# Performance work log

Hardware: AMD Instinct MI355X
Metric: run time of the kernel (lower is better)

## Reference

```python
import jax, jax.numpy as jnp
import numpy as np

B, S, D, H, DFF, L = 32, 512, 512, 8, 2048, 3
DK = D // H
NEG = -1e32


def _ln(x, g, b):
    m = jnp.mean(x, axis=-1, keepdims=True)
    v = jnp.mean((x - m) ** 2, axis=-1, keepdims=True)
    return (x - m) / jnp.sqrt(v + 1e-5) * g + b


def _mha(query, key, value, mask, zero_pad, gam, Wk, bk, Wv, bv, Wo, bo):
    # kq_same: q and k both use k_linear
    q = (query @ Wk + bk).reshape(B, S, H, DK).transpose(0, 2, 1, 3)
    k = (key @ Wk + bk).reshape(B, S, H, DK).transpose(0, 2, 1, 3)
    v = (value @ Wv + bv).reshape(B, S, H, DK).transpose(0, 2, 1, 3)
    scores = jnp.einsum('bhid,bhjd->bhij', q, k) / jnp.sqrt(jnp.float32(DK))
    # distance-decay rescoring (no-grad in original)
    p = jax.nn.softmax(jnp.where(mask, scores, NEG), axis=-1) * mask
    distcum = jnp.cumsum(p, axis=-1)
    disttotal = jnp.sum(p, axis=-1, keepdims=True)
    idx = jnp.arange(S)
    pos = jnp.abs(idx[None, :] - idx[:, None]).astype(jnp.float32)  # [S,S]
    dist = jax.lax.stop_gradient(
        jnp.sqrt(jnp.clip((disttotal - distcum) * pos[None, None], 0.0, None)))
    gamma = -jax.nn.softplus(gam)[None, :, None, None]  # [1,H,1,1]
    total_effect = jnp.clip(jnp.exp(dist * gamma), 1e-5, 1e5)
    scores = jnp.where(mask, scores * total_effect, NEG)
    scores = jax.nn.softmax(scores, axis=-1)
    if zero_pad:
        scores = scores * (idx[:, None] > 0)[None, None, :, :].astype(scores.dtype) * 0 + \
                 scores * (idx > 0).astype(scores.dtype)[None, None, :, None]
    out = jnp.einsum('bhij,bhjd->bhid', scores, v)
    out = out.transpose(0, 2, 1, 3).reshape(B, S, D)
    return out @ Wo + bo


def _layer(i, mask, zero_pad, query, key, values, apply_pos,
           Wk, bk, Wv, bv, Wo, bo, gammas, ln1_g, ln1_b, W1, b1, W2, b2, ln2_g, ln2_b):
    a = _mha(query, key, values, mask, zero_pad, gammas[i],
             Wk[i], bk[i], Wv[i], bv[i], Wo[i], bo[i])
    x = _ln(query + a, ln1_g[i], ln1_b[i])
    if apply_pos:
        f = jax.nn.relu(x @ W1[i] + b1[i]) @ W2[i] + b2[i]
        x = _ln(x + f, ln2_g[i], ln2_b[i])
    return x


def setup_inputs() -> dict:
    key = jax.random.key(0)
    ks = jax.random.split(key, 12)
    sc = 0.02
    inp = {
        'q_embed_data': jax.random.normal(ks[0], (B, S, D), jnp.float32),
        'qa_embed_data': jax.random.normal(ks[1], (B, S, D), jnp.float32),
        'Wk': jax.random.normal(ks[2], (L, D, D), jnp.float32) * sc,
        'bk': jnp.zeros((L, D), jnp.float32),
        'Wv': jax.random.normal(ks[3], (L, D, D), jnp.float32) * sc,
        'bv': jnp.zeros((L, D), jnp.float32),
        'Wo': jax.random.normal(ks[4], (L, D, D), jnp.float32) * sc,
        'bo': jnp.zeros((L, D), jnp.float32),
        'gammas': jax.random.normal(ks[5], (L, H), jnp.float32) * 0.5,
        'ln1_g': jnp.ones((L, D), jnp.float32),
        'ln1_b': jnp.zeros((L, D), jnp.float32),
        'W1': jax.random.normal(ks[6], (L, D, DFF), jnp.float32) * sc,
        'b1': jnp.zeros((L, DFF), jnp.float32),
        'W2': jax.random.normal(ks[7], (L, DFF, D), jnp.float32) * sc,
        'b2': jnp.zeros((L, D), jnp.float32),
        'ln2_g': jnp.ones((L, D), jnp.float32),
        'ln2_b': jnp.zeros((L, D), jnp.float32),
    }
    return inp


def reference(q_embed_data, qa_embed_data, Wk, bk, Wv, bv, Wo, bo, gammas,
              ln1_g, ln1_b, W1, b1, W2, b2, ln2_g, ln2_b):
    P = (Wk, bk, Wv, bv, Wo, bo, gammas, ln1_g, ln1_b, W1, b1, W2, b2, ln2_g, ln2_b)
    mask1 = jnp.tril(jnp.ones((S, S), bool), 0)[None, None]   # peek current+past
    mask0 = jnp.tril(jnp.ones((S, S), bool), -1)[None, None]  # peek only past
    y = qa_embed_data
    x = q_embed_data
    # blocks_1 (n_blocks=1): mask=1, self-attn, apply_pos
    y = _layer(0, mask1, False, y, y, y, True, *P)
    # blocks_2 (2 layers): first mask=1 no FFN, second mask=0 zero_pad cross-attn to y
    x = _layer(1, mask1, False, x, x, x, False, *P)
    x = _layer(2, mask0, True, x, x, y, True, *P)
    return x
```

## Files before the change

kernel.cpp:

```cpp
#include <hip/hip_runtime.h>

#define BB   32
#define SS   512
#define DDIM 512
#define HH   8
#define DFFN 2048
#define MR   (BB*SS)

typedef unsigned int   u32;
typedef unsigned short u16;
typedef unsigned char  u8;
typedef __attribute__((ext_vector_type(8))) short bf16x8;
typedef __attribute__((ext_vector_type(4))) float f32x4;

__device__ __forceinline__ u32 packbf2(float x, float y) {
  u32 ux = __float_as_uint(x), uy = __float_as_uint(y);
  u32 hx = (ux + 0x7FFFu + ((ux >> 16) & 1u)) >> 16;
  u32 hy = (uy + 0x7FFFu + ((uy >> 16) & 1u)) >> 16;
  return hx | (hy << 16);
}
__device__ __forceinline__ u16 pack1bf(float x) {
  u32 u = __float_as_uint(x);
  return (u16)((u + 0x7FFFu + ((u >> 16) & 1u)) >> 16);
}

__device__ __forceinline__ float redsum2(float v) {
  v += __shfl_xor(v, 16, 64);
  v += __shfl_xor(v, 32, 64);
  return v;
}

#if __has_builtin(__builtin_amdgcn_exp2f)
__device__ __forceinline__ float ex2c(float x) { return __builtin_amdgcn_exp2f(fminf(x, 110.f)); }
__device__ __forceinline__ float ex2r(float x) { return __builtin_amdgcn_exp2f(x); }
#else
__device__ __forceinline__ float ex2c(float x) {
  float r = fminf(x, 110.f);
  asm("v_exp_f32 %0, %1" : "=v"(r) : "v"(r));
  return r;
}
__device__ __forceinline__ float ex2r(float x) {
  float r;
  asm("v_exp_f32 %0, %1" : "=v"(r) : "v"(x));
  return r;
}
#endif

__global__ __launch_bounds__(256) void pack_flat2(
    const float* __restrict__ in0, const float* __restrict__ in1,
    u16* __restrict__ out0, u16* __restrict__ out1) {
  const float* in = blockIdx.y ? in1 : in0;
  u16* out = blockIdx.y ? out1 : out0;
  size_t i = ((size_t)blockIdx.x * 256 + threadIdx.x) * 8;
  float4 a = *(const float4*)(in + i);
  float4 b = *(const float4*)(in + i + 4);
  uint4 o;
  o.x = packbf2(a.x, a.y); o.y = packbf2(a.z, a.w);
  o.z = packbf2(b.x, b.y); o.w = packbf2(b.z, b.w);
  *(uint4*)(out + i) = o;
}

__device__ __forceinline__ void wtp_body(const float* __restrict__ in,
                                         u16* __restrict__ out, int K, int N,
                                         int bx, int by) {
  __shared__ float tile[64][65];
  const int t  = threadIdx.x;
  const int n0 = bx * 64, k0 = by * 64;
  #pragma unroll
  for (int it = 0; it < 4; ++it) {
    int idx = it * 256 + t;
    int kk = idx >> 4, n4 = idx & 15;
    float4 v = *(const float4*)(in + (size_t)(k0 + kk) * N + n0 + n4 * 4);
    tile[kk][n4*4+0] = v.x; tile[kk][n4*4+1] = v.y;
    tile[kk][n4*4+2] = v.z; tile[kk][n4*4+3] = v.w;
  }
  __syncthreads();
  #pragma unroll
  for (int it = 0; it < 4; ++it) {
    int idx = it * 256 + t;
    int nn = idx >> 4, g = idx & 15;
    uint2 o;
    o.x = packbf2(tile[g*4+0][nn], tile[g*4+1][nn]);
    o.y = packbf2(tile[g*4+2][nn], tile[g*4+3][nn]);
    *(uint2*)(out + (size_t)(n0 + nn) * K + k0 + g * 4) = o;
  }
}
__global__ __launch_bounds__(256) void pack_w_t(const float* __restrict__ in,
                                                u16* __restrict__ out, int K, int N) {
  wtp_body(in + (size_t)blockIdx.z * K * N, out + (size_t)blockIdx.z * N * K,
           K, N, blockIdx.x, blockIdx.y);
}
__global__ __launch_bounds__(256) void pack_w_sq(
    const float* __restrict__ Wk, const float* __restrict__ Wv,
    const float* __restrict__ Wo,
    u16* __restrict__ WkT, u16* __restrict__ WvT, u16* __restrict__ WoT) {
  const int z = blockIdx.z, which = z / 3, li = z % 3;
  const float* in = (which == 0 ? Wk : which == 1 ? Wv : Wo) + (size_t)li * 262144;
  u16* out = (which == 0 ? WkT : which == 1 ? WvT : WoT) + (size_t)li * 262144;
  wtp_body(in, out, 512, 512, blockIdx.x, blockIdx.y);
}

struct GJob { const u16* A; const u16* Bt; const float* bias;
              float* outF; u16* outB; float sc; };
struct GJobs { GJob j[4]; };

__global__ __launch_bounds__(512, 2) void gemm8(
    GJobs jobs, int lda, int ldb, int ldc, int Kz, int relu)
{
  __shared__ __align__(16) u8 lds[131072];

  const GJob J = jobs.j[blockIdx.z];
  const u16* A    = J.A;
  const u16* Bt   = J.Bt;
  const float* bias = J.bias;
  float* outF = J.outF;
  u16*   outB = J.outB;
  const float sc = J.sc;

  const int nwg  = gridDim.x * gridDim.y;
  const int orig = blockIdx.y * gridDim.x + blockIdx.x;
  const int q8   = nwg >> 3, r8 = nwg & 7;
  const int xcd  = orig & 7, idx8 = orig >> 3;
  const int wg   = (xcd < r8 ? xcd * (q8 + 1) : r8 * (q8 + 1) + (xcd - r8) * q8) + idx8;
  const int bx   = wg % gridDim.x, by = wg / gridDim.x;
  const int row0 = by * 256, col0 = bx * 256;

  const int t    = threadIdx.x;
  const int lane = t & 63, wid = t >> 6;
  const int wm   = wid >> 2, wn = wid & 3;
  const int rl   = lane & 15, kg = lane >> 4;

  const int NT = Kz >> 6;

  f32x4 acc[8][4] = {};

  auto stageA = [&](int buf, int h, int kt) {
    #pragma unroll
    for (int l = 0; l < 2; ++l) {
      int s  = (l * 512 + t) >> 3;
      int kb = ((lane & 7) * 16) ^ ((s & 7) << 4);
      int row = row0 + ((s >> 6) * 128) + h * 64 + (s & 63);
      const u8* src = (const u8*)A + (size_t)row * lda * 2 + (size_t)kt * 128 + kb;
      u8* dst = lds + buf * 65536 + h * 16384 + (l * 512 + wid * 64) * 16;
      __builtin_amdgcn_global_load_lds(
          (const __attribute__((address_space(1))) u32*)src,
          (__attribute__((address_space(3))) u32*)dst, 16, 0, 0);
    }
  };
  auto stageB = [&](int buf, int h, int kt) {
    #pragma unroll
    for (int l = 0; l < 2; ++l) {
      int s  = (l * 512 + t) >> 3;
      int kb = ((lane & 7) * 16) ^ ((s & 7) << 4);
      int col = col0 + ((s >> 5) * 64) + h * 32 + (s & 31);
      const u8* src = (const u8*)Bt + (size_t)col * ldb * 2 + (size_t)kt * 128 + kb;
      u8* dst = lds + buf * 65536 + 32768 + h * 16384 + (l * 512 + wid * 64) * 16;
      __builtin_amdgcn_global_load_lds(
          (const __attribute__((address_space(1))) u32*)src,
          (__attribute__((address_space(3))) u32*)dst, 16, 0, 0);
    }
  };

  auto rdA = [&](int buf, int mh, int m, int ks) -> bf16x8 {
    int s = wm * 64 + m * 16 + rl;
    int off = buf * 65536 + mh * 16384 + s * 128 + (((ks * 32 + kg * 8) * 2) ^ ((s & 7) << 4));
    return *(const bf16x8*)(lds + off);
  };
  auto rdB = [&](int buf, int nh, int n, int ks) -> bf16x8 {
    int s = wn * 32 + n * 16 + rl;
    int off = buf * 65536 + 32768 + nh * 16384 + s * 128 + (((ks * 32 + kg * 8) * 2) ^ ((s & 7) << 4));
    return *(const bf16x8*)(lds + off);
  };

#define GBAR asm volatile("s_barrier" ::: "memory")
#define VMW4 asm volatile("s_waitcnt vmcnt(4)" ::: "memory")
#define VMW0 asm volatile("s_waitcnt vmcnt(0)" ::: "memory")

#define PHASE(BUF, MH, NH, STAGECODE, DOVM) do {                               \
    bf16x8 af_[4][2], bf_[2][2];                                               \
    _Pragma("unroll") for (int m_ = 0; m_ < 4; ++m_)                           \
      _Pragma("unroll") for (int k_ = 0; k_ < 2; ++k_)                         \
        af_[m_][k_] = rdA(BUF, MH, m_, k_);                                    \
    _Pragma("unroll") for (int n_ = 0; n_ < 2; ++n_)                           \
      _Pragma("unroll") for (int k_ = 0; k_ < 2; ++k_)                         \
        bf_[n_][k_] = rdB(BUF, NH, n_, k_);                                    \
    STAGECODE;                                                                 \
    if (DOVM == 1) VMW4;                                                       \
    if (DOVM == 2) VMW0;                                                       \
    GBAR;                                                                      \
    __builtin_amdgcn_s_setprio(1);                                             \
    _Pragma("unroll") for (int m_ = 0; m_ < 4; ++m_)                           \
      _Pragma("unroll") for (int n_ = 0; n_ < 2; ++n_) {                       \
        acc[(MH)*4+m_][(NH)*2+n_] = __builtin_amdgcn_mfma_f32_16x16x32_bf16(   \
            af_[m_][0], bf_[n_][0], acc[(MH)*4+m_][(NH)*2+n_], 0, 0, 0);       \
        acc[(MH)*4+m_][(NH)*2+n_] = __builtin_amdgcn_mfma_f32_16x16x32_bf16(   \
            af_[m_][1], bf_[n_][1], acc[(MH)*4+m_][(NH)*2+n_], 0, 0, 0);       \
      }                                                                        \
    __builtin_amdgcn_s_setprio(0);                                             \
    GBAR;                                                                      \
  } while (0)

  stageA(0, 0, 0); stageB(0, 0, 0); stageA(0, 1, 0); stageB(0, 1, 0);
  stageA(1, 0, 1); stageB(1, 0, 1);
  VMW4; GBAR;

  for (int i = 0; i < (NT >> 1) - 1; ++i) {
    const int T1 = 2 * i + 1, T2 = 2 * i + 2, T3 = 2 * i + 3;
    PHASE(0, 0, 0, stageA(1, 1, T1), 0);
    PHASE(0, 0, 1, stageB(1, 1, T1), 0);
    PHASE(0, 1, 0, stageA(0, 0, T2), 0);
    PHASE(0, 1, 1, stageB(0, 0, T2), 1);
    PHASE(1, 0, 0, stageA(0, 1, T2), 0);
    PHASE(1, 0, 1, stageB(0, 1, T2), 0);
    PHASE(1, 1, 0, stageA(1, 0, T3), 0);
    PHASE(1, 1, 1, stageB(1, 0, T3), 1);
  }
  PHASE(0, 0, 0, stageA(1, 1, NT - 1), 0);
  PHASE(0, 0, 1, stageB(1, 1, NT - 1), 0);
  PHASE(0, 1, 0, ;, 0);
  PHASE(0, 1, 1, ;, 2);
  PHASE(1, 0, 0, ;, 0);
  PHASE(1, 0, 1, ;, 0);
  PHASE(1, 1, 0, ;, 0);
  PHASE(1, 1, 1, ;, 0);
#undef PHASE
#undef GBAR
#undef VMW4
#undef VMW0

  #pragma unroll
  for (int M = 0; M < 8; ++M) {
    #pragma unroll
    for (int N2 = 0; N2 < 4; ++N2) {
      const int col = col0 + wn * 64 + N2 * 16 + rl;
      const float bs = bias ? bias[col] : 0.f;
      #pragma unroll
      for (int q = 0; q < 4; ++q) {
        const int row = row0 + wm * 128 + M * 16 + kg * 4 + q;
        float v = (acc[M][N2][q] + bs) * sc;
        if (relu) v = fmaxf(v, 0.f);
        if (outF) outF[(size_t)row * ldc + col] = v;
        if (outB) outB[(size_t)row * ldc + col] = pack1bf(v);
      }
    }
  }
}

__global__ __attribute__((amdgpu_flat_work_group_size(1024, 1024)))
void attn_mfma(
    const u16* __restrict__ qkA, const u16* __restrict__ vbA,
    const float* __restrict__ gmA, u16* __restrict__ outAp,
    const u16* __restrict__ qkB, const u16* __restrict__ vbB,
    const float* __restrict__ gmB, u16* __restrict__ outBp,
    int nA, int mask_excl, int zero_pad)
{
  __shared__ __align__(16) u8 kSb[65536];
  __shared__ __align__(16) u8 vTb[65536];
  __shared__ __align__(16) u8 pChb[16384];

  const int t    = threadIdx.x;
  const int lane = t & 63, wid = t >> 6;
  const int ql   = lane & 15, g = lane >> 4;
  const int bid  = blockIdx.x;
  const int sel  = bid >= nA;
  const u16* qk    = sel ? qkB : qkA;
  const u16* vbuf  = sel ? vbB : vbA;
  const float* gam = sel ? gmB : gmA;
  u16* out         = sel ? outBp : outAp;
  const int bh = sel ? bid - nA : bid;
  const int b = bh >> 3, h = bh & 7;
  const size_t base = (size_t)b * SS * DDIM + (size_t)h * 64;

  float gv = gam[h];
  float sp = (gv > 0.f) ? (gv + log1pf(__expf(-gv))) : log1pf(__expf(gv));
  const float gamma2 = -sp * 1.442695041f;

  for (int it = 0; it < 4; ++it) {
    int idx = it * 1024 + t;
    int j = idx >> 3, u = idx & 7;
    uint4 w = *(const uint4*)(qk + base + (size_t)j * DDIM + u * 8);
    *(uint4*)(kSb + ((j * 128 + u * 16) ^ ((j & 7) << 4))) = w;
  }
  for (int it = 0; it < 2; ++it) {
    int idx = it * 1024 + t;
    int jp = idx >> 3, u = idx & 7;
    const u16* src = vbuf + base + (size_t)(2 * jp) * DDIM + u * 8;
    uint4 r0 = *(const uint4*)src;
    uint4 r1 = *(const uint4*)(src + DDIM);
    const u16* a0 = (const u16*)&r0;
    const u16* a1 = (const u16*)&r1;
    #pragma unroll
    for (int dd = 0; dd < 8; ++dd) {
      int d = u * 8 + dd;
      u32 w = (u32)a0[dd] | ((u32)a1[dd] << 16);
      *(u32*)(vTb + d * 1024 + ((4 * jp) ^ ((dd ^ u) << 4))) = w;
    }
  }
  __syncthreads();

  bool vm[4];
  #pragma unroll
  for (int rg = 0; rg < 4; ++rg) {
    int kl = 4 * g + rg;
    vm[rg] = mask_excl ? (kl < ql) : (kl <= ql);
  }

  u8* pB = pChb + wid * 1024;
  const int swp = (ql & 7) << 4;

  int vbase[4], vsw[4];
  #pragma unroll
  for (int n = 0; n < 4; ++n) {
    int d = n * 16 + ql;
    vbase[n] = d * 1024;
    vsw[n]   = ((d & 7) ^ ((d >> 3) & 7)) << 4;
  }

  #pragma unroll
  for (int ri = 0; ri < 2; ++ri) {
    const int rs = __builtin_amdgcn_readfirstlane(ri ? (31 - wid) : wid);
    const int i0 = rs * 16;

    const int qrow = i0 + ql;
    const int qsw  = (qrow & 7) << 4;
    bf16x8 qf0 = *(const bf16x8*)(kSb + ((qrow * 128      + g * 16) ^ qsw));
    bf16x8 qf1 = *(const bf16x8*)(kSb + ((qrow * 128 + 64 + g * 16) ^ qsw));

    float S1l = 0.f;
    #pragma unroll
    for (int kt = 0; kt < 32; ++kt) {
      if (kt <= rs) {
        const bool dg = (kt == rs);
        const int krow = kt * 16 + ql;
        const int ksw  = (krow & 7) << 4;
        bf16x8 ka0 = *(const bf16x8*)(kSb + ((krow * 128      + g * 16) ^ ksw));
        bf16x8 ka1 = *(const bf16x8*)(kSb + ((krow * 128 + 64 + g * 16) ^ ksw));
        f32x4 dv = {};
        dv = __builtin_amdgcn_mfma_f32_16x16x32_bf16(ka0, qf0, dv, 0, 0, 0);
        dv = __builtin_amdgcn_mfma_f32_16x16x32_bf16(ka1, qf1, dv, 0, 0, 0);
        float e0 = (!dg || vm[0]) ? ex2c(dv[0]) : 0.f;
        float e1 = (!dg || vm[1]) ? ex2c(dv[1]) : 0.f;
        float e2 = (!dg || vm[2]) ? ex2c(dv[2]) : 0.f;
        float e3 = (!dg || vm[3]) ? ex2c(dv[3]) : 0.f;
        S1l += (e0 + e1) + (e2 + e3);
      }
    }
    const float S1   = redsum2(S1l);
    const float inv1 = (S1 > 0.f) ? (1.f / S1) : 0.f;

    f32x4 oacc[4] = {};
    float cbase = 0.f, S2l = 0.f;
    const float qlf = (float)(i0 + ql);

    auto subkt = [&](int kt, bool dg, u32& wA, u32& wB) {
      const int krow = kt * 16 + ql;
      const int ksw  = (krow & 7) << 4;
      bf16x8 ka0 = *(const bf16x8*)(kSb + ((krow * 128      + g * 16) ^ ksw));
      bf16x8 ka1 = *(const bf16x8*)(kSb + ((krow * 128 + 64 + g * 16) ^ ksw));
      f32x4 dv = {};
      dv = __builtin_amdgcn_mfma_f32_16x16x32_bf16(ka0, qf0, dv, 0, 0, 0);
      dv = __builtin_amdgcn_mfma_f32_16x16x32_bf16(ka1, qf1, dv, 0, 0, 0);
      const bool v0 = !dg || vm[0], v1 = !dg || vm[1];
      const bool v2 = !dg || vm[2], v3 = !dg || vm[3];
      float e0 = v0 ? ex2c(dv[0]) : 0.f;
      float e1 = v1 ? ex2c(dv[1]) : 0.f;
      float e2 = v2 ? ex2c(dv[2]) : 0.f;
      float e3 = v3 ? ex2c(dv[3]) : 0.f;
      float p0 = e0, p1 = p0 + e1, p2 = p1 + e2, p3 = p2 + e3;
      float bq  = __shfl_xor(p3, 16, 64);
      float s1p = p3 + bq;
      float cq  = __shfl_xor(s1p, 32, 64);
      float gp  = ((g & 1) ? bq : 0.f) + ((g & 2) ? cq : 0.f);
      float tt  = s1p + cq;
      const float pbase = cbase + gp;
      const float pf = qlf - (float)(kt * 16 + 4 * g);
      float ipr[4] = {p0, p1, p2, p3};
      bool  vv[4]  = {v0, v1, v2, v3};
      float sv[4]  = {dv[0], dv[1], dv[2], dv[3]};
      float q2[4];
      #pragma unroll
      for (int rg = 0; rg < 4; ++rg) {
        float rem  = fmaxf((S1 - (pbase + ipr[rg])) * inv1, 0.f);
        float pos  = pf - (float)rg;
        float dist = sqrtf(rem * pos);
        float eff  = fmaxf(ex2r(gamma2 * dist), 1e-5f);
        float ee   = vv[rg] ? ex2c(sv[rg] * eff) : 0.f;
        q2[rg] = ee;
        S2l += ee;
      }
      wA = packbf2(q2[0], q2[1]);
      wB = packbf2(q2[2], q2[3]);
      cbase += tt;
    };

    #pragma unroll
    for (int c = 0; c < 16; ++c) {
      if (2 * c <= rs) {
        u32 w0 = 0, w1 = 0, w2 = 0, w3 = 0;
        subkt(2 * c, (2 * c == rs), w0, w1);
        if (2 * c + 1 <= rs) subkt(2 * c + 1, (2 * c + 1 == rs), w2, w3);
        *(u32*)(pB + ((ql * 64 +      8 * g    ) ^ swp)) = w0;
        *(u32*)(pB + ((ql * 64 +      8 * g + 4) ^ swp)) = w1;
        *(u32*)(pB + ((ql * 64 + 32 + 8 * g    ) ^ swp)) = w2;
        *(u32*)(pB + ((ql * 64 + 32 + 8 * g + 4) ^ swp)) = w3;
        bf16x8 pa = *(const bf16x8*)(pB + ((ql * 64 + 16 * g) ^ swp));
        #pragma unroll
        for (int n = 0; n < 4; ++n) {
          bf16x8 vb = *(const bf16x8*)(vTb + vbase[n] + ((64 * c + 16 * g) ^ vsw[n]));
          oacc[n] = __builtin_amdgcn_mfma_f32_16x16x32_bf16(pa, vb, oacc[n], 0, 0, 0);
        }
      }
    }

    const float S2   = redsum2(S2l);
    const float inv2 = 1.f / fmaxf(S2, 1e-30f);
    float i2[4];
    #pragma unroll
    for (int rg = 0; rg < 4; ++rg) i2[rg] = __shfl(inv2, 4 * g + rg, 64);

    #pragma unroll
    for (int n = 0; n < 4; ++n) {
      #pragma unroll
      for (int rg = 0; rg < 4; ++rg) {
        const int qo = i0 + 4 * g + rg;
        float val = oacc[n][rg] * i2[rg];
        if (zero_pad && qo == 0) val = 0.f;
        out[base + (size_t)qo * DDIM + n * 16 + ql] = pack1bf(val);
      }
    }
  }
}

struct LNJob { const u16* a; const u16* b; const u16* c;
               const float* g; const float* be; float* outF; u16* outB; };
struct LNJobs { LNJob j[2]; };

__global__ __launch_bounds__(256) void ln_kernel(LNJobs jobs)
{
  const LNJob J = jobs.j[blockIdx.y];
  const int lane = threadIdx.x & 63, w = threadIdx.x >> 6;
  const size_t row = (size_t)blockIdx.x * 4 + w;
  const size_t off8 = row * DDIM + lane * 8;

  uint4 ab = *(const uint4*)(J.a + off8);
  uint4 bb = *(const uint4*)(J.b + off8);
  const u16* ap = (const u16*)&ab;
  const u16* bp = (const u16*)&bb;
  float v[8];
  #pragma unroll
  for (int k = 0; k < 8; ++k)
    v[k] = __uint_as_float(((u32)ap[k]) << 16) + __uint_as_float(((u32)bp[k]) << 16);
  if (J.c) {
    uint4 cb = *(const uint4*)(J.c + off8);
    const u16* cp = (const u16*)&cb;
    #pragma unroll
    for (int k = 0; k < 8; ++k) v[k] += __uint_as_float(((u32)cp[k]) << 16);
  }

  float sum = 0.f;
  #pragma unroll
  for (int k = 0; k < 8; ++k) sum += v[k];
  #pragma unroll
  for (int off = 32; off > 0; off >>= 1) sum += __shfl_xor(sum, off, 64);
  const float mean = sum * (1.f / 512.f);
  float var = 0.f;
  #pragma unroll
  for (int k = 0; k < 8; ++k) { float dd = v[k] - mean; var = fmaf(dd, dd, var); }
  #pragma unroll
  for (int off = 32; off > 0; off >>= 1) var += __shfl_xor(var, off, 64);
  var *= (1.f / 512.f);
  const float inv = rsqrtf(var + 1e-5f);

  float4 g0 = *(const float4*)(J.g + lane * 8);
  float4 g1 = *(const float4*)(J.g + lane * 8 + 4);
  float4 e0 = *(const float4*)(J.be + lane * 8);
  float4 e1 = *(const float4*)(J.be + lane * 8 + 4);
  float gv[8] = {g0.x, g0.y, g0.z, g0.w, g1.x, g1.y, g1.z, g1.w};
  float ev[8] = {e0.x, e0.y, e0.z, e0.w, e1.x, e1.y, e1.z, e1.w};
  float o[8];
  #pragma unroll
  for (int k = 0; k < 8; ++k) o[k] = (v[k] - mean) * inv * gv[k] + ev[k];

  if (J.outF) {
    float4 f0 = {o[0], o[1], o[2], o[3]};
    float4 f1 = {o[4], o[5], o[6], o[7]};
    *(float4*)(J.outF + off8)     = f0;
    *(float4*)(J.outF + off8 + 4) = f1;
  }
  if (J.outB) {
    uint4 p;
    p.x = packbf2(o[0], o[1]); p.y = packbf2(o[2], o[3]);
    p.z = packbf2(o[4], o[5]); p.w = packbf2(o[6], o[7]);
    *(uint4*)(J.outB + off8) = p;
  }
}

extern "C" void kernel_launch(void* const* d_in, const int* in_sizes, int n_in,
                              void* d_out, int out_size, void* d_ws, size_t ws_size,
                              hipStream_t stream) {
  const float* qe  = (const float*)d_in[0];
  const float* qa  = (const float*)d_in[1];
  const float* Wk  = (const float*)d_in[2];
  const float* bk  = (const float*)d_in[3];
  const float* Wv  = (const float*)d_in[4];
  const float* bv  = (const float*)d_in[5];
  const float* Wo  = (const float*)d_in[6];
  const float* bo  = (const float*)d_in[7];
  const float* gm  = (const float*)d_in[8];
  const float* l1g = (const float*)d_in[9];
  const float* l1b = (const float*)d_in[10];
  const float* W1  = (const float*)d_in[11];
  const float* b1  = (const float*)d_in[12];
  const float* W2  = (const float*)d_in[13];
  const float* b2  = (const float*)d_in[14];
  const float* l2g = (const float*)d_in[15];
  const float* l2b = (const float*)d_in[16];

  char* ws = (char*)d_ws;
  u16* WT  = (u16*)ws;
  u16* A0  = (u16*)(ws + ((size_t)18  << 20));
  u16* A1  = (u16*)(ws + ((size_t)34  << 20));
  u16* A2  = (u16*)(ws + ((size_t)50  << 20));
  u16* A3  = (u16*)(ws + ((size_t)66  << 20));
  u16* A4  = (u16*)(ws + ((size_t)82  << 20));
  u16* A5  = (u16*)(ws + ((size_t)98  << 20));
  u16* B0  = (u16*)(ws + ((size_t)114 << 20));
  u16* B1  = (u16*)(ws + ((size_t)130 << 20));
  u16* X0  = (u16*)(ws + ((size_t)146 << 20));
  u16* Amid = A2;

  u16* WkT = WT;
  u16* WvT = WT + (size_t)3 * 262144;
  u16* WoT = WT + (size_t)6 * 262144;
  u16* W1T = WT + (size_t)9 * 262144;
  u16* W2T = W1T + (size_t)3 * 1048576;

  pack_w_sq<<<dim3(8, 8, 9),  256, 0, stream>>>(Wk, Wv, Wo, WkT, WvT, WoT);
  pack_w_t<<<dim3(32, 8, 3), 256, 0, stream>>>(W1, W1T, 512, 2048);
  pack_w_t<<<dim3(8, 32, 3), 256, 0, stream>>>(W2, W2T, 2048, 512);
  pack_flat2<<<dim3(4096, 2), 256, 0, stream>>>(qa, qe, A0, A1);

  const float SQ2 = 0.4246609001f;

  auto g8 = [&](GJobs jobs, int lda, int ldb, int ldc,
                int M, int N, int Kz, int relu, int nz) {
    gemm8<<<dim3(N / 256, M / 256, nz), 512, 0, stream>>>(
        jobs, lda, ldb, ldc, Kz, relu);
  };
  auto ln2x = [&](LNJobs jobs, int nz) {
    ln_kernel<<<dim3(MR / 4, nz), 256, 0, stream>>>(jobs);
  };

  auto WkT_l = [&](int l){ return WkT + (size_t)l * 262144; };
  auto WvT_l = [&](int l){ return WvT + (size_t)l * 262144; };
  auto WoT_l = [&](int l){ return WoT + (size_t)l * 262144; };
  auto W1T_l = [&](int l){ return W1T + (size_t)l * 1048576; };
  auto W2T_l = [&](int l){ return W2T + (size_t)l * 1048576; };

  {
    GJobs pj = {{ {A0, WkT_l(0), bk,       nullptr, A2, SQ2},
                  {A0, WvT_l(0), bv,       nullptr, A3, 1.f},
                  {A1, WkT_l(1), bk + 512, nullptr, A4, SQ2},
                  {A1, WvT_l(1), bv + 512, nullptr, A5, 1.f} }};
    g8(pj, 512, 512, 512, MR, 512, 512, 0, 4);

    attn_mfma<<<BB * HH * 2, 1024, 0, stream>>>(
        A2, A3, gm, A3, A4, A5, gm + HH, A5, BB * HH, 0, 0);

    GJobs wj = {{ {A3, WoT_l(0), bo,       nullptr, B0, 1.f},
                  {A5, WoT_l(1), bo + 512, nullptr, B1, 1.f},
                  {}, {} }};
    g8(wj, 512, 512, 512, MR, 512, 512, 0, 2);

    LNJobs lj = {{ {A0, B0, nullptr, l1g,       l1b,       nullptr, X0},
                   {A1, B1, nullptr, l1g + 512, l1b + 512, nullptr, A1} }};
    ln2x(lj, 2);
  }
  {
    GJobs w1j = {{ {X0, W1T_l(0), b1, nullptr, Amid, 1.f}, {}, {}, {} }};
    g8(w1j, 512, 512, 2048, MR, 2048, 512, 1, 1);
    GJobs w2j = {{ {Amid,        W2T_l(0),        b2,      nullptr, B0, 1.f},
                   {Amid + 1024, W2T_l(0) + 1024, nullptr, nullptr, B1, 1.f},
                   {}, {} }};
    g8(w2j, 2048, 2048, 512, MR, 512, 1024, 0, 2);
    LNJobs lj = {{ {X0, B0, B1, l2g, l2b, nullptr, A0}, {} }};
    ln2x(lj, 1);
  }
  {
    GJobs pj = {{ {A1, WkT_l(2), bk + 1024, nullptr, A2, SQ2},
                  {A0, WvT_l(2), bv + 1024, nullptr, A3, 1.f},
                  {}, {} }};
    g8(pj, 512, 512, 512, MR, 512, 512, 0, 2);

    attn_mfma<<<BB * HH, 1024, 0, stream>>>(
        A2, A3, gm + 2 * HH, A3, A2, A3, gm + 2 * HH, A3, BB * HH, 1, 1);

    GJobs wj = {{ {A3,       WoT_l(2),       bo + 1024, nullptr, B0, 1.f},
                  {A3 + 256, WoT_l(2) + 256, nullptr,   nullptr, B1, 1.f},
                  {}, {} }};
    g8(wj, 512, 512, 512, MR, 512, 256, 0, 2);

    LNJobs l1j = {{ {A1, B0, B1, l1g + 1024, l1b + 1024, nullptr, A1}, {} }};
    ln2x(l1j, 1);

    GJobs w1j = {{ {A1, W1T_l(2), b1 + 2 * DFFN, nullptr, Amid, 1.f}, {}, {}, {} }};
    g8(w1j, 512, 512, 2048, MR, 2048, 512, 1, 1);
    GJobs w2j = {{ {Amid,        W2T_l(2),        b2 + 1024, nullptr, B0, 1.f},
                   {Amid + 1024, W2T_l(2) + 1024, nullptr,   nullptr, B1, 1.f},
                   {}, {} }};
    g8(w2j, 2048, 2048, 512, MR, 512, 1024, 0, 2);

    LNJobs l2j = {{ {A1, B0, B1, l2g + 1024, l2b + 1024, (float*)d_out, nullptr}, {} }};
    ln2x(l2j, 1);
  }
}
```

Measured before the change: 603.7 us.

## Switch GEMM to 32x32x16 MFMA with K-split B staging layout

Replaces the 16x16x32 bf16 MFMA tiles in the GEMM kernel with 32x32x16 tiles, accumulating into 16-wide float vectors per tile. The B-operand staging layout changes so each LDS half holds a K-half for all 256 columns rather than a column half, with a new swizzle, and the phase loop now iterates over K halves instead of N halves. Larger MFMA tiles cut the number of LDS fragment reads per FLOP and the instruction count. The cost is a reworked epilogue row mapping and new LDS bank-conflict behaviour from the different swizzle.

```diff
diff --git a/kernel.cpp b/kernel.cpp
--- a/kernel.cpp
+++ b/kernel.cpp
@@ -10,8 +10,9 @@
 typedef unsigned int   u32;
 typedef unsigned short u16;
 typedef unsigned char  u8;
-typedef __attribute__((ext_vector_type(8))) short bf16x8;
-typedef __attribute__((ext_vector_type(4))) float f32x4;
+typedef __attribute__((ext_vector_type(8)))  short bf16x8;
+typedef __attribute__((ext_vector_type(4)))  float f32x4;
+typedef __attribute__((ext_vector_type(16))) float f32x16;
 
 __device__ __forceinline__ u32 packbf2(float x, float y) {
   u32 ux = __float_as_uint(x), uy = __float_as_uint(y);
@@ -128,11 +129,11 @@
   const int t    = threadIdx.x;
   const int lane = t & 63, wid = t >> 6;
   const int wm   = wid >> 2, wn = wid & 3;
-  const int rl   = lane & 15, kg = lane >> 4;
+  const int rl   = lane & 31, lhi = lane >> 5;
 
   const int NT = Kz >> 6;
 
-  f32x4 acc[8][4] = {};
+  f32x16 acc[4][2] = {};
 
   auto stageA = [&](int buf, int h, int kt) {
     #pragma unroll
@@ -150,10 +151,10 @@
   auto stageB = [&](int buf, int h, int kt) {
     #pragma unroll
     for (int l = 0; l < 2; ++l) {
-      int s  = (l * 512 + t) >> 3;
-      int kb = ((lane & 7) * 16) ^ ((s & 7) << 4);
-      int col = col0 + ((s >> 5) * 64) + h * 32 + (s & 31);
-      const u8* src = (const u8*)Bt + (size_t)col * ldb * 2 + (size_t)kt * 128 + kb;
+      int idx = l * 512 + t;
+      int c  = idx >> 2, jj = idx & 3;
+      int j  = jj ^ (c & 3);
+      const u16* src = Bt + (size_t)(col0 + c) * ldb + kt * 64 + h * 32 + j * 8;
       u8* dst = lds + buf * 65536 + 32768 + h * 16384 + (l * 512 + wid * 64) * 16;
       __builtin_amdgcn_global_load_lds(
           (const __attribute__((address_space(1))) u32*)src,
@@ -161,14 +162,16 @@
     }
   };
 
-  auto rdA = [&](int buf, int mh, int m, int ks) -> bf16x8 {
-    int s = wm * 64 + m * 16 + rl;
-    int off = buf * 65536 + mh * 16384 + s * 128 + (((ks * 32 + kg * 8) * 2) ^ ((s & 7) << 4));
+  auto rdA = [&](int buf, int mh, int mt, int kh, int q) -> bf16x8 {
+    int s = wm * 64 + mt * 32 + rl;
+    int off = buf * 65536 + mh * 16384 + s * 128 +
+              (((kh * 64 + q * 32 + lhi * 16)) ^ ((s & 7) << 4));
     return *(const bf16x8*)(lds + off);
   };
-  auto rdB = [&](int buf, int nh, int n, int ks) -> bf16x8 {
-    int s = wn * 32 + n * 16 + rl;
-    int off = buf * 65536 + 32768 + nh * 16384 + s * 128 + (((ks * 32 + kg * 8) * 2) ^ ((s & 7) << 4));
+  auto rdB = [&](int buf, int kh, int nt, int q) -> bf16x8 {
+    int c = wn * 64 + nt * 32 + rl;
+    int off = buf * 65536 + 32768 + kh * 16384 + c * 64 +
+              (((q * 2 + lhi) ^ (c & 3)) * 16);
     return *(const bf16x8*)(lds + off);
   };
 
@@ -176,25 +179,25 @@
 #define VMW4 asm volatile("s_waitcnt vmcnt(4)" ::: "memory")
 #define VMW0 asm volatile("s_waitcnt vmcnt(0)" ::: "memory")
 
-#define PHASE(BUF, MH, NH, STAGECODE, DOVM) do {                               \
-    bf16x8 af_[4][2], bf_[2][2];                                               \
-    _Pragma("unroll") for (int m_ = 0; m_ < 4; ++m_)                           \
-      _Pragma("unroll") for (int k_ = 0; k_ < 2; ++k_)                         \
-        af_[m_][k_] = rdA(BUF, MH, m_, k_);                                    \
-    _Pragma("unroll") for (int n_ = 0; n_ < 2; ++n_)                           \
-      _Pragma("unroll") for (int k_ = 0; k_ < 2; ++k_)                         \
-        bf_[n_][k_] = rdB(BUF, NH, n_, k_);                                    \
+#define PHASE(BUF, MH, KH, STAGECODE, DOVM) do {                               \
+    bf16x8 af_[2][2], bf_[2][2];                                               \
+    _Pragma("unroll") for (int mt_ = 0; mt_ < 2; ++mt_)                        \
+      _Pragma("unroll") for (int q_ = 0; q_ < 2; ++q_)                         \
+        af_[mt_][q_] = rdA(BUF, MH, mt_, KH, q_);                              \
+    _Pragma("unroll") for (int nt_ = 0; nt_ < 2; ++nt_)                        \
+      _Pragma("unroll") for (int q_ = 0; q_ < 2; ++q_)                         \
+        bf_[nt_][q_] = rdB(BUF, KH, nt_, q_);                                  \
     STAGECODE;                                                                 \
     if (DOVM == 1) VMW4;                                                       \
     if (DOVM == 2) VMW0;                                                       \
     GBAR;                                                                      \
     __builtin_amdgcn_s_setprio(1);                                             \
-    _Pragma("unroll") for (int m_ = 0; m_ < 4; ++m_)                           \
-      _Pragma("unroll") for (int n_ = 0; n_ < 2; ++n_) {                       \
-        acc[(MH)*4+m_][(NH)*2+n_] = __builtin_amdgcn_mfma_f32_16x16x32_bf16(   \
-            af_[m_][0], bf_[n_][0], acc[(MH)*4+m_][(NH)*2+n_], 0, 0, 0);       \
-        acc[(MH)*4+m_][(NH)*2+n_] = __builtin_amdgcn_mfma_f32_16x16x32_bf16(   \
-            af_[m_][1], bf_[n_][1], acc[(MH)*4+m_][(NH)*2+n_], 0, 0, 0);       \
+    _Pragma("unroll") for (int mt_ = 0; mt_ < 2; ++mt_)                        \
+      _Pragma("unroll") for (int nt_ = 0; nt_ < 2; ++nt_) {                    \
+        acc[(MH)*2+mt_][nt_] = __builtin_amdgcn_mfma_f32_32x32x16_bf16(        \
+            af_[mt_][0], bf_[nt_][0], acc[(MH)*2+mt_][nt_], 0, 0, 0);          \
+        acc[(MH)*2+mt_][nt_] = __builtin_amdgcn_mfma_f32_32x32x16_bf16(        \
+            af_[mt_][1], bf_[nt_][1], acc[(MH)*2+mt_][nt_], 0, 0, 0);          \
       }                                                                        \
     __builtin_amdgcn_s_setprio(0);                                             \
     GBAR;                                                                      \
@@ -229,15 +232,15 @@
 #undef VMW0
 
   #pragma unroll
-  for (int M = 0; M < 8; ++M) {
-    #pragma unroll
-    for (int N2 = 0; N2 < 4; ++N2) {
-      const int col = col0 + wn * 64 + N2 * 16 + rl;
+  for (int mi = 0; mi < 4; ++mi) {
+    #pragma unroll
+    for (int nt = 0; nt < 2; ++nt) {
+      const int col = col0 + wn * 64 + nt * 32 + rl;
       const float bs = bias ? bias[col] : 0.f;
       #pragma unroll
-      for (int q = 0; q < 4; ++q) {
-        const int row = row0 + wm * 128 + M * 16 + kg * 4 + q;
-        float v = (acc[M][N2][q] + bs) * sc;
+      for (int reg = 0; reg < 16; ++reg) {
+        const int row = row0 + wm * 128 + mi * 32 + (reg & 3) + 8 * (reg >> 2) + 4 * lhi;
+        float v = (acc[mi][nt][reg] + bs) * sc;
         if (relu) v = fmaxf(v, 0.f);
         if (outF) outF[(size_t)row * ldc + col] = v;
         if (outB) outB[(size_t)row * ldc + col] = pack1bf(v);
```

After: 601.2 us. About the same (-0.4%).
